# Kernel optimization log

Hardware: AMD Instinct MI355X
Metric: run time of the kernel (lower is better)

The kernel has to match this reference:

```python
import jax, jax.numpy as jnp
import numpy as np

N_NODES = 50000
N_EDGES = 800000
IN_F, HID_F, OUT_F = 256, 128, 64
NEG_SLOPE = 0.2
EPS = 1e-16


def _aggregate_with_attention(x, src, tgt, a_w, a_b, num_nodes):
    # x: [N, d]; src/tgt: [E]; a_w: [2d]; a_b: [1]
    d = x.shape[-1]
    x_src = x[src]                                   # [E, d] gather
    # att(cat([x_src, x_tgt])) == x_src @ a_w[:d] + x_tgt @ a_w[d:] + b
    alpha = x_src @ a_w[:d] + x[tgt] @ a_w[d:] + a_b[0]   # [E]
    alpha = jnp.where(alpha >= 0, alpha, NEG_SLOPE * alpha)  # leaky_relu(0.2)
    # segment softmax over edges grouped by target node
    m = jax.ops.segment_max(alpha, tgt, num_segments=num_nodes)   # [N]
    e = jnp.exp(alpha - m[tgt])                                    # [E]
    s = jax.ops.segment_sum(e, tgt, num_segments=num_nodes)       # [N]
    alpha = e / (s[tgt] + EPS)                                     # [E]
    msgs = x_src * alpha[:, None]                                  # [E, d]
    return jax.ops.segment_sum(msgs, tgt, num_segments=num_nodes)  # [N, d]


def setup_inputs() -> dict:
    key = jax.random.key(0)
    ks = jax.random.split(key, 10)
    x = jax.random.normal(ks[0], (N_NODES, IN_F), dtype=jnp.float32)
    edge_index = jax.random.randint(ks[1], (2, N_EDGES), 0, N_NODES, dtype=jnp.int32)
    sc1 = 1.0 / np.sqrt(IN_F)
    sc2 = 1.0 / np.sqrt(HID_F)
    return {
        "x": x,
        "edge_index": edge_index,
        "W1": jax.random.normal(ks[2], (IN_F, HID_F), dtype=jnp.float32) * sc1,
        "b1": jax.random.normal(ks[3], (HID_F,), dtype=jnp.float32) * sc1,
        "a1_w": jax.random.normal(ks[4], (2 * HID_F,), dtype=jnp.float32) * sc2,
        "a1_b": jax.random.normal(ks[5], (1,), dtype=jnp.float32) * sc2,
        "W2": jax.random.normal(ks[6], (HID_F, OUT_F), dtype=jnp.float32) * sc2,
        "b2": jax.random.normal(ks[7], (OUT_F,), dtype=jnp.float32) * sc2,
        "a2_w": jax.random.normal(ks[8], (2 * OUT_F,), dtype=jnp.float32) * (1.0 / np.sqrt(OUT_F)),
        "a2_b": jax.random.normal(ks[9], (1,), dtype=jnp.float32) * (1.0 / np.sqrt(OUT_F)),
    }


def reference(x, edge_index, W1, b1, a1_w, a1_b, W2, b2, a2_w, a2_b):
    src, tgt = edge_index[0], edge_index[1]
    n = x.shape[0]
    # eval mode: dropout is identity
    h = jax.nn.elu(x @ W1 + b1)                           # [N, HID]
    h = _aggregate_with_attention(h, src, tgt, a1_w, a1_b, n)
    o = h @ W2 + b2                                        # [N, OUT]
    o = _aggregate_with_attention(o, src, tgt, a2_w, a2_b, n)
    return jax.nn.log_softmax(o, axis=-1)
```

## Files before the change

kernel.cpp:

```cpp
#include <hip/hip_runtime.h>

#define NN    50000
#define NE    800000
#define INF_  256
#define HIDF  128
#define OUTF  64
#define NBUCK 196
#define CAP   5120
#define CHUNK 2048
#define NPART1 ((NE + CHUNK - 1) / CHUNK)
#define NLIN1B ((NN + 127) / 128)
#define NLIN2B ((NN + 127) / 128)
#define NPREP  160

typedef unsigned int uint;
typedef unsigned short ushort;
typedef __attribute__((ext_vector_type(8))) short short8;
typedef __attribute__((ext_vector_type(4))) float float4v;

__device__ __forceinline__ short f2bf(float f) {
    union { float f; unsigned u; } v; v.f = f;
    unsigned r = v.u + 0x7fffu + ((v.u >> 16) & 1u);
    return (short)(r >> 16);
}
__device__ __forceinline__ float bflo(uint u) {
    union { uint u; float f; } v; v.u = u << 16; return v.f;
}
__device__ __forceinline__ float bfhi(uint u) {
    union { uint u; float f; } v; v.u = u & 0xffff0000u; return v.f;
}

__device__ __forceinline__ int excl_scan256(int v, int* ws) {
    int lane = threadIdx.x & 63, wv = threadIdx.x >> 6;
    int x = v;
    #pragma unroll
    for (int o = 1; o < 64; o <<= 1) {
        int y = __shfl_up(x, o);
        if (lane >= o) x += y;
    }
    if (lane == 63) ws[wv] = x;
    __syncthreads();
    int add = 0;
    #pragma unroll
    for (int w = 0; w < 4; w++) add += (w < wv) ? ws[w] : 0;
    return x + add - v;
}

__device__ __forceinline__ int excl_scan512(int v, int* ws) {
    int lane = threadIdx.x & 63, wv = threadIdx.x >> 6;
    int x = v;
    #pragma unroll
    for (int o = 1; o < 64; o <<= 1) {
        int y = __shfl_up(x, o);
        if (lane >= o) x += y;
    }
    if (lane == 63) ws[wv] = x;
    __syncthreads();
    int add = 0;
    #pragma unroll
    for (int w = 0; w < 8; w++) add += (w < wv) ? ws[w] : 0;
    return x + add - v;
}

__global__ __launch_bounds__(256) void k_prep(const float* __restrict__ W1, const float* __restrict__ W2,
                                              short* __restrict__ W1f, short* __restrict__ W2f,
                                              int* __restrict__ bcur) {
    if (blockIdx.x == NPREP) {
        if (threadIdx.x < NBUCK) bcur[threadIdx.x] = 0;
        return;
    }
    int i = blockIdx.x * 256 + threadIdx.x;
    if (i < INF_ * HIDF) {
        int kk = i & 7, t = i >> 3;
        int m_l = t & 15, q = (t >> 4) & 3, s = t >> 6;
        int nb = s & 7, kc = s >> 3;
        int k = kc * 32 + q * 8 + kk, n = nb * 16 + m_l;
        W1f[i] = f2bf(W1[k * HIDF + n]);
    } else if (i < INF_ * HIDF + HIDF * OUTF) {
        int i2 = i - INF_ * HIDF;
        int kk = i2 & 7, t = i2 >> 3;
        int m_l = t & 15, q = (t >> 4) & 3, s = t >> 6;
        int nb = s & 3, kc = s >> 2;
        int k = kc * 32 + q * 8 + kk, n = nb * 16 + m_l;
        W2f[i2] = f2bf(W2[k * OUTF + n]);
    }
}


__global__ __launch_bounds__(256, 3) void k_f1(const int* __restrict__ src, const int* __restrict__ tgt,
                                               int* __restrict__ bcur, uint2* __restrict__ pairs,
                                               const float* __restrict__ X, const short* __restrict__ W1f,
                                               const float* __restrict__ b1, ushort* __restrict__ Hb,
                                               const float* __restrict__ a1w, float* __restrict__ s1s,
                                               float* __restrict__ s1t) {
    if (blockIdx.x < NPART1) {
        __shared__ int hist[NBUCK], lofs[NBUCK], cur[NBUCK], gstart[NBUCK];
        __shared__ int ws[4];
        __shared__ int ltgt[CHUNK], lsrc[CHUNK];
        int tid = threadIdx.x;
        for (int i = tid; i < NBUCK; i += 256) hist[i] = 0;
        __syncthreads();

        int base = blockIdx.x * CHUNK;
        int cnt = NE - base; if (cnt > CHUNK) cnt = CHUNK;

        int t_[8], s_[8];
        #pragma unroll
        for (int k = 0; k < 8; k++) {
            int idx = k * 256 + tid;
            if (idx < cnt) {
                int j = base + idx;
                t_[k] = tgt[j]; s_[k] = src[j];
                atomicAdd(&hist[t_[k] >> 8], 1);
            } else t_[k] = -1;
        }
        __syncthreads();

        int v = (tid < NBUCK) ? hist[tid] : 0;
        int excl = excl_scan256(v, ws);
        if (tid < NBUCK) {
            lofs[tid] = excl;
            cur[tid] = excl;
            gstart[tid] = atomicAdd(&bcur[tid], v);
        }
        __syncthreads();

        #pragma unroll
        for (int k = 0; k < 8; k++) {
            if (t_[k] >= 0) {
                int b = t_[k] >> 8;
                int pos = atomicAdd(&cur[b], 1);
                ltgt[pos] = t_[k]; lsrc[pos] = s_[k];
            }
        }
        __syncthreads();

        for (int j = tid; j < cnt; j += 256) {
            int tv = ltgt[j];
            int b = tv >> 8;
            int dst = gstart[b] + (j - lofs[b]);
            pairs[(size_t)b * CAP + dst] = make_uint2((uint)tv, (uint)lsrc[j]);
        }
        return;
    }
    int bid = blockIdx.x - NPART1;
    int w = threadIdx.x >> 6;
    int l = threadIdx.x & 63;
    int m_l = l & 15, q = l >> 4;
    int row0 = bid * 128 + w * 32;
    int rA0 = row0 + m_l;
    int rA1 = row0 + 16 + m_l;
    int rc0 = rA0 < NN ? rA0 : NN - 1;
    int rc1 = rA1 < NN ? rA1 : NN - 1;
    const float* pa0 = X + (size_t)rc0 * INF_ + q * 8;
    const float* pa1 = X + (size_t)rc1 * INF_ + q * 8;
    const short8* Bp = (const short8*)W1f;

    short8 af0[8], af1[8];
    #pragma unroll
    for (int kc = 0; kc < 8; kc++) {
        float4 u0 = *(const float4*)(pa0 + kc * 32);
        float4 u1 = *(const float4*)(pa0 + kc * 32 + 4);
        float4 v0 = *(const float4*)(pa1 + kc * 32);
        float4 v1 = *(const float4*)(pa1 + kc * 32 + 4);
        af0[kc][0] = f2bf(u0.x); af0[kc][1] = f2bf(u0.y); af0[kc][2] = f2bf(u0.z); af0[kc][3] = f2bf(u0.w);
        af0[kc][4] = f2bf(u1.x); af0[kc][5] = f2bf(u1.y); af0[kc][6] = f2bf(u1.z); af0[kc][7] = f2bf(u1.w);
        af1[kc][0] = f2bf(v0.x); af1[kc][1] = f2bf(v0.y); af1[kc][2] = f2bf(v0.z); af1[kc][3] = f2bf(v0.w);
        af1[kc][4] = f2bf(v1.x); af1[kc][5] = f2bf(v1.y); af1[kc][6] = f2bf(v1.z); af1[kc][7] = f2bf(v1.w);
    }

    float4v acc0[8] = {}, acc1[8] = {};
    #pragma unroll
    for (int kc = 0; kc < 8; kc++) {
        #pragma unroll
        for (int n = 0; n < 8; n++) {
            short8 b = Bp[(kc * 8 + n) * 64 + l];
            acc0[n] = __builtin_amdgcn_mfma_f32_16x16x32_bf16(af0[kc], b, acc0[n], 0, 0, 0);
            acc1[n] = __builtin_amdgcn_mfma_f32_16x16x32_bf16(af1[kc], b, acc1[n], 0, 0, 0);
        }
    }

    float vs_r[8], vt_r[8];
    #pragma unroll
    for (int r = 0; r < 8; r++) { vs_r[r] = 0.f; vt_r[r] = 0.f; }
    #pragma unroll
    for (int n = 0; n < 8; n++) {
        int col = n * 16 + m_l;
        float bias = b1[col];
        float aw0 = a1w[col], aw1 = a1w[HIDF + col];
        #pragma unroll
        for (int r = 0; r < 4; r++) {
            int row = row0 + q * 4 + r;
            float v = acc0[n][r] + bias;
            v = v > 0.f ? v : expm1f(v);
            vs_r[r] += v * aw0; vt_r[r] += v * aw1;
            if (row < NN) Hb[(size_t)row * HIDF + col] = (ushort)f2bf(v);

            int row1 = row0 + 16 + q * 4 + r;
            float v1 = acc1[n][r] + bias;
            v1 = v1 > 0.f ? v1 : expm1f(v1);
            vs_r[4 + r] += v1 * aw0; vt_r[4 + r] += v1 * aw1;
            if (row1 < NN) Hb[(size_t)row1 * HIDF + col] = (ushort)f2bf(v1);
        }
    }
    #pragma unroll
    for (int r = 0; r < 8; r++) {
        #pragma unroll
        for (int o = 1; o < 16; o <<= 1) {
            vs_r[r] += __shfl_xor(vs_r[r], o);
            vt_r[r] += __shfl_xor(vt_r[r], o);
        }
    }
    if (m_l == 0) {
        #pragma unroll
        for (int r = 0; r < 4; r++) {
            int row = row0 + q * 4 + r;
            if (row < NN) { s1s[row] = vs_r[r]; s1t[row] = vt_r[r]; }
            int row1 = row0 + 16 + q * 4 + r;
            if (row1 < NN) { s1s[row1] = vs_r[4 + r]; s1t[row1] = vt_r[4 + r]; }
        }
    }
}

__global__ __launch_bounds__(512) void k_part2(const int* __restrict__ bcur, const uint2* __restrict__ pairs,
                                               int* __restrict__ fsrc, int* __restrict__ nbeg,
                                               int* __restrict__ ncnt) {
    __shared__ int hist[256], cur[256];
    __shared__ int ws[8];
    int tid = threadIdx.x;
    int b = blockIdx.x;
    int cnt = __builtin_amdgcn_readfirstlane(bcur[b]);
    if (tid < 256) hist[tid] = 0;
    __syncthreads();

    const uint2* pb = pairs + (size_t)b * CAP;
    for (int j = tid; j < cnt; j += 512) {
        uint2 e = pb[j];
        atomicAdd(&hist[e.x & 255], 1);
    }
    __syncthreads();

    int v = (tid < 256) ? hist[tid] : 0;
    int excl = excl_scan512(v, ws);
    if (tid < 256) {
        int node = (b << 8) + tid;
        if (node < NN) { nbeg[node] = b * CAP + excl; ncnt[node] = v; }
        cur[tid] = excl;
    }
    __syncthreads();

    for (int j = tid; j < cnt; j += 512) {
        uint2 e = pb[j];
        int pos = atomicAdd(&cur[e.x & 255], 1);
        fsrc[(size_t)b * CAP + pos] = (int)e.y;
    }
}

__global__ __launch_bounds__(256, 3) void k_linear2(const short* __restrict__ Hin, const short* __restrict__ W2f,
                                                    const float* __restrict__ b2, ushort* __restrict__ Ob,
                                                    const float* __restrict__ a2w, float* __restrict__ s2s,
                                                    float* __restrict__ s2t) {
    int w = threadIdx.x >> 6;
    int l = threadIdx.x & 63;
    int m_l = l & 15, q = l >> 4;
    int row0 = blockIdx.x * 128 + w * 32;
    int rA0 = row0 + m_l;
    int rA1 = row0 + 16 + m_l;
    int rc0 = rA0 < NN ? rA0 : NN - 1;
    int rc1 = rA1 < NN ? rA1 : NN - 1;
    const short* pa0 = Hin + (size_t)rc0 * HIDF + q * 8;
    const short* pa1 = Hin + (size_t)rc1 * HIDF + q * 8;
    const short8* Bp = (const short8*)W2f;

    short8 af0[4], af1[4];
    #pragma unroll
    for (int kc = 0; kc < 4; kc++) {
        af0[kc] = *(const short8*)(pa0 + kc * 32);
        af1[kc] = *(const short8*)(pa1 + kc * 32);
    }

    float4v acc0[4] = {}, acc1[4] = {};
    #pragma unroll
    for (int kc = 0; kc < 4; kc++) {
        #pragma unroll
        for (int n = 0; n < 4; n++) {
            short8 b = Bp[(kc * 4 + n) * 64 + l];
            acc0[n] = __builtin_amdgcn_mfma_f32_16x16x32_bf16(af0[kc], b, acc0[n], 0, 0, 0);
            acc1[n] = __builtin_amdgcn_mfma_f32_16x16x32_bf16(af1[kc], b, acc1[n], 0, 0, 0);
        }
    }

    float vs_r[8], vt_r[8];
    #pragma unroll
    for (int r = 0; r < 8; r++) { vs_r[r] = 0.f; vt_r[r] = 0.f; }
    #pragma unroll
    for (int n = 0; n < 4; n++) {
        int col = n * 16 + m_l;
        float bias = b2[col];
        float aw0 = a2w[col], aw1 = a2w[OUTF + col];
        #pragma unroll
        for (int r = 0; r < 4; r++) {
            int row = row0 + q * 4 + r;
            float v = acc0[n][r] + bias;
            vs_r[r] += v * aw0; vt_r[r] += v * aw1;
            if (row < NN) Ob[(size_t)row * OUTF + col] = (ushort)f2bf(v);

            int row1 = row0 + 16 + q * 4 + r;
            float v1 = acc1[n][r] + bias;
            vs_r[4 + r] += v1 * aw0; vt_r[4 + r] += v1 * aw1;
            if (row1 < NN) Ob[(size_t)row1 * OUTF + col] = (ushort)f2bf(v1);
        }
    }
    #pragma unroll
    for (int r = 0; r < 8; r++) {
        #pragma unroll
        for (int o = 1; o < 16; o <<= 1) {
            vs_r[r] += __shfl_xor(vs_r[r], o);
            vt_r[r] += __shfl_xor(vt_r[r], o);
        }
    }
    if (m_l == 0) {
        #pragma unroll
        for (int r = 0; r < 4; r++) {
            int row = row0 + q * 4 + r;
            if (row < NN) { s2s[row] = vs_r[r]; s2t[row] = vt_r[r]; }
            int row1 = row0 + 16 + q * 4 + r;
            if (row1 < NN) { s2s[row1] = vs_r[4 + r]; s2t[row1] = vt_r[4 + r]; }
        }
    }
}


__global__ __launch_bounds__(256) void k_agg1f(const uint* __restrict__ Hb4, const int* __restrict__ nbeg,
                                               const int* __restrict__ ncnt, const int* __restrict__ fsrc,
                                               const float* __restrict__ ss, const float* __restrict__ st_,
                                               const float* __restrict__ ab, uint* __restrict__ Hagg4) {
    int wid  = (blockIdx.x * 256 + threadIdx.x) >> 6;
    int lane = threadIdx.x & 63;
    if (wid >= NN) return;
    int beg = __builtin_amdgcn_readfirstlane(nbeg[wid]);
    int deg = __builtin_amdgcn_readfirstlane(ncnt[wid]);
    int end = beg + deg;
    float bias = ab[0] + st_[wid];
    float ax = 0.f, ay = 0.f, bx = 0.f, by = 0.f;

    if (deg > 0 && deg <= 64) {
        int my_s = 0; float a = -INFINITY;
        if (lane < deg) {
            my_s = fsrc[beg + lane];
            float t = ss[my_s] + bias;
            a = t >= 0.f ? t : 0.2f * t;
        }
        float m = a;
        #pragma unroll
        for (int o = 32; o > 0; o >>= 1) m = fmaxf(m, __shfl_xor(m, o));
        float e = (lane < deg) ? __expf(a - m) : 0.f;
        float sum = e;
        #pragma unroll
        for (int o = 32; o > 0; o >>= 1) sum += __shfl_xor(sum, o);
        float p = e * (1.f / (sum + 1e-16f));
        int nfull8 = deg & ~7;
        int j = 0;
        if (nfull8 > 0) {
            float wA[8]; uint xA[8];
            #pragma unroll
            for (int u = 0; u < 8; u++) {
                int s = __shfl(my_s, u); wA[u] = __shfl(p, u);
                xA[u] = Hb4[(size_t)s * 64 + lane];
            }
            for (j = 8; j < nfull8; j += 8) {
                float wB[8]; uint xB[8];
                #pragma unroll
                for (int u = 0; u < 8; u++) {
                    int s = __shfl(my_s, j + u); wB[u] = __shfl(p, j + u);
                    xB[u] = Hb4[(size_t)s * 64 + lane];
                }
                #pragma unroll
                for (int u = 0; u < 8; u += 2) {
                    ax += wA[u] * bflo(xA[u]);         ay += wA[u] * bfhi(xA[u]);
                    bx += wA[u + 1] * bflo(xA[u + 1]); by += wA[u + 1] * bfhi(xA[u + 1]);
                }
                #pragma unroll
                for (int u = 0; u < 8; u++) { xA[u] = xB[u]; wA[u] = wB[u]; }
            }
            #pragma unroll
            for (int u = 0; u < 8; u += 2) {
                ax += wA[u] * bflo(xA[u]);         ay += wA[u] * bfhi(xA[u]);
                bx += wA[u + 1] * bflo(xA[u + 1]); by += wA[u + 1] * bfhi(xA[u + 1]);
            }
        }
        if (j < deg) {
            int rem = deg - j;
            int sA[8]; float wA[8]; uint xA[8];
            #pragma unroll
            for (int u = 0; u < 8; u++) { sA[u] = __shfl(my_s, j + u); wA[u] = __shfl(p, j + u); }
            #pragma unroll
            for (int u = 0; u < 8; u++) xA[u] = (u < rem) ? Hb4[(size_t)sA[u] * 64 + lane] : 0u;
            #pragma unroll
            for (int u = 0; u < 8; u += 2) {
                ax += wA[u] * bflo(xA[u]);         ay += wA[u] * bfhi(xA[u]);
                bx += wA[u + 1] * bflo(xA[u + 1]); by += wA[u + 1] * bfhi(xA[u + 1]);
            }
        }
    } else if (deg > 64) {
        float m = -INFINITY;
        for (int i = beg + lane; i < end; i += 64) {
            float t = ss[fsrc[i]] + bias;
            t = t >= 0.f ? t : 0.2f * t;
            m = fmaxf(m, t);
        }
        #pragma unroll
        for (int o = 32; o > 0; o >>= 1) m = fmaxf(m, __shfl_xor(m, o));
        float sum = 0.f;
        for (int i = beg + lane; i < end; i += 64) {
            float t = ss[fsrc[i]] + bias;
            t = t >= 0.f ? t : 0.2f * t;
            sum += __expf(t - m);
        }
        #pragma unroll
        for (int o = 32; o > 0; o >>= 1) sum += __shfl_xor(sum, o);
        float inv = 1.f / (sum + 1e-16f);
        for (int c = beg; c < end; c += 64) {
            int cnt = min(64, end - c);
            int my_s = 0; float p = 0.f;
            if (lane < cnt) {
                my_s = fsrc[c + lane];
                float t = ss[my_s] + bias;
                t = t >= 0.f ? t : 0.2f * t;
                p = __expf(t - m) * inv;
            }
            for (int j = 0; j < cnt; j += 4) {
                int s0 = __shfl(my_s, j),     s1 = __shfl(my_s, j + 1);
                int s2 = __shfl(my_s, j + 2), s3 = __shfl(my_s, j + 3);
                float w0 = __shfl(p, j),     w1 = __shfl(p, j + 1);
                float w2 = __shfl(p, j + 2), w3 = __shfl(p, j + 3);
                uint x0 = Hb4[(size_t)s0 * 64 + lane];
                uint x1 = Hb4[(size_t)s1 * 64 + lane];
                uint x2 = Hb4[(size_t)s2 * 64 + lane];
                uint x3 = Hb4[(size_t)s3 * 64 + lane];
                ax += w0 * bflo(x0); ay += w0 * bfhi(x0);
                bx += w1 * bflo(x1); by += w1 * bfhi(x1);
                ax += w2 * bflo(x2); ay += w2 * bfhi(x2);
                bx += w3 * bflo(x3); by += w3 * bfhi(x3);
            }
        }
    }
    float fx = ax + bx, fy = ay + by;
    uint outv = (uint)(ushort)f2bf(fx) | ((uint)(ushort)f2bf(fy) << 16);
    Hagg4[(size_t)wid * 64 + lane] = outv;
}

__global__ __launch_bounds__(256) void k_agg2f(const uint* __restrict__ Ob4, const int* __restrict__ nbeg,
                                               const int* __restrict__ ncnt, const int* __restrict__ fsrc,
                                               const float* __restrict__ ss, const float* __restrict__ st_,
                                               const float* __restrict__ ab, float* __restrict__ out) {
    int wid  = (blockIdx.x * 256 + threadIdx.x) >> 6;
    int lane = threadIdx.x & 63;
    if (wid >= NN) return;
    int half = lane >> 5, li = lane & 31;
    int beg = __builtin_amdgcn_readfirstlane(nbeg[wid]);
    int deg = __builtin_amdgcn_readfirstlane(ncnt[wid]);
    int end = beg + deg;
    float bias = ab[0] + st_[wid];
    float a0 = 0.f, a1 = 0.f;

    if (deg > 0 && deg <= 64) {
        int my_s = 0; float a = -INFINITY;
        if (lane < deg) {
            my_s = fsrc[beg + lane];
            float t = ss[my_s] + bias;
            a = t >= 0.f ? t : 0.2f * t;
        }
        float m = a;
        #pragma unroll
        for (int o = 32; o > 0; o >>= 1) m = fmaxf(m, __shfl_xor(m, o));
        float e = (lane < deg) ? __expf(a - m) : 0.f;
        float sum = e;
        #pragma unroll
        for (int o = 32; o > 0; o >>= 1) sum += __shfl_xor(sum, o);
        float p = e * (1.f / (sum + 1e-16f));
        int nfull8 = deg & ~7;
        int j = 0;
        if (nfull8 > 0) {
            float wA_[4]; uint xA_[4];
            #pragma unroll
            for (int u = 0; u < 4; u++) {
                int ei_ = 2 * u + half;
                int s = __shfl(my_s, ei_); wA_[u] = __shfl(p, ei_);
                xA_[u] = Ob4[(size_t)s * 32 + li];
            }
            for (j = 8; j < nfull8; j += 8) {
                float wB_[4]; uint xB_[4];
                #pragma unroll
                for (int u = 0; u < 4; u++) {
                    int ei_ = j + 2 * u + half;
                    int s = __shfl(my_s, ei_); wB_[u] = __shfl(p, ei_);
                    xB_[u] = Ob4[(size_t)s * 32 + li];
                }
                #pragma unroll
                for (int u = 0; u < 4; u++) { a0 += wA_[u] * bflo(xA_[u]); a1 += wA_[u] * bfhi(xA_[u]); }
                #pragma unroll
                for (int u = 0; u < 4; u++) { xA_[u] = xB_[u]; wA_[u] = wB_[u]; }
            }
            #pragma unroll
            for (int u = 0; u < 4; u++) { a0 += wA_[u] * bflo(xA_[u]); a1 += wA_[u] * bfhi(xA_[u]); }
        }
        if (j < deg) {
            int rem = deg - j;
            #pragma unroll
            for (int k = 0; k < 4; k++) {
                int eo = 2 * k + half;
                int ei_ = j + eo;
                int sx = __shfl(my_s, ei_);
                float wx = __shfl(p, ei_);
                uint xx = (eo < rem) ? Ob4[(size_t)sx * 32 + li] : 0u;
                a0 += wx * bflo(xx); a1 += wx * bfhi(xx);
            }
        }
    } else if (deg > 64) {
        float m = -INFINITY;
        for (int i = beg + lane; i < end; i += 64) {
            float t = ss[fsrc[i]] + bias;
            t = t >= 0.f ? t : 0.2f * t;
            m = fmaxf(m, t);
        }
        #pragma unroll
        for (int o = 32; o > 0; o >>= 1) m = fmaxf(m, __shfl_xor(m, o));
        float sum = 0.f;
        for (int i = beg + lane; i < end; i += 64) {
            float t = ss[fsrc[i]] + bias;
            t = t >= 0.f ? t : 0.2f * t;
            sum += __expf(t - m);
        }
        #pragma unroll
        for (int o = 32; o > 0; o >>= 1) sum += __shfl_xor(sum, o);
        float inv = 1.f / (sum + 1e-16f);
        for (int c = beg; c < end; c += 64) {
            int cnt = min(64, end - c);
            int my_s = 0; float p = 0.f;
            if (lane < cnt) {
                my_s = fsrc[c + lane];
                float t = ss[my_s] + bias;
                t = t >= 0.f ? t : 0.2f * t;
                p = __expf(t - m) * inv;
            }
            for (int j = 0; j < cnt; j += 4) {
                int e0 = j + half, e1 = j + 2 + half;
                int s0 = __shfl(my_s, e0), s1 = __shfl(my_s, e1);
                float w0 = __shfl(p, e0), w1 = __shfl(p, e1);
                uint x0 = Ob4[(size_t)s0 * 32 + li];
                uint x1 = Ob4[(size_t)s1 * 32 + li];
                a0 += w0 * bflo(x0); a1 += w0 * bfhi(x0);
                a0 += w1 * bflo(x1); a1 += w1 * bfhi(x1);
            }
        }
    }
    a0 += __shfl_xor(a0, 32);
    a1 += __shfl_xor(a1, 32);
    float mx = fmaxf(a0, a1);
    #pragma unroll
    for (int o = 16; o > 0; o >>= 1) mx = fmaxf(mx, __shfl_xor(mx, o));
    float es = __expf(a0 - mx) + __expf(a1 - mx);
    #pragma unroll
    for (int o = 16; o > 0; o >>= 1) es += __shfl_xor(es, o);
    float lg = __logf(es);
    if (half == 0) {
        float2 r; r.x = a0 - mx - lg; r.y = a1 - mx - lg;
        ((float2*)out)[(size_t)wid * 32 + li] = r;
    }
}


extern "C" void kernel_launch(void* const* d_in, const int* in_sizes, int n_in,
                              void* d_out, int out_size, void* d_ws, size_t ws_size,
                              hipStream_t stream) {
    const float* X   = (const float*)d_in[0];
    const int*   ei  = (const int*)d_in[1];
    const float* W1  = (const float*)d_in[2];
    const float* b1  = (const float*)d_in[3];
    const float* a1w = (const float*)d_in[4];
    const float* a1b = (const float*)d_in[5];
    const float* W2  = (const float*)d_in[6];
    const float* b2  = (const float*)d_in[7];
    const float* a2w = (const float*)d_in[8];
    const float* a2b = (const float*)d_in[9];
    const int* src = ei;
    const int* tgt = ei + NE;

    char* p = (char*)d_ws;
    size_t off = 0;
    auto alloc = [&](size_t bytes) -> char* {
        char* r = p + off;
        off = (off + bytes + 255) & ~(size_t)255;
        return r;
    };
    ushort* Hb    = (ushort*)alloc((size_t)NN * HIDF * 2);
    ushort* Hagg  = (ushort*)alloc((size_t)NN * HIDF * 2);
    ushort* Ob    = (ushort*)alloc((size_t)NN * OUTF * 2);
    short* W1f    = (short*)alloc((size_t)INF_ * HIDF * 2);
    short* W2f    = (short*)alloc((size_t)HIDF * OUTF * 2);
    float* s1s    = (float*)alloc((size_t)NN * 4);
    float* s1t    = (float*)alloc((size_t)NN * 4);
    float* s2s    = (float*)alloc((size_t)NN * 4);
    float* s2t    = (float*)alloc((size_t)NN * 4);
    int*   bcur   = (int*)alloc((size_t)NBUCK * 4);
    uint2* pairs  = (uint2*)alloc((size_t)NBUCK * CAP * 8);
    int*   fsrc   = (int*)alloc((size_t)NBUCK * CAP * 4);
    int*   nbeg   = (int*)alloc((size_t)NN * 4);
    int*   ncnt   = (int*)alloc((size_t)NN * 4);

    k_prep   <<<NPREP + 1, 256, 0, stream>>>(W1, W2, W1f, W2f, bcur);
    k_f1     <<<NPART1 + NLIN1B, 256, 0, stream>>>(src, tgt, bcur, pairs,
                                                   X, W1f, b1, Hb, a1w, s1s, s1t);
    k_part2  <<<NBUCK, 512, 0, stream>>>(bcur, pairs, fsrc, nbeg, ncnt);
    k_agg1f  <<<NN / 4, 256, 0, stream>>>((const uint*)Hb, nbeg, ncnt, fsrc, s1s, s1t, a1b, (uint*)Hagg);
    k_linear2<<<NLIN2B, 256, 0, stream>>>((const short*)Hagg, W2f, b2, Ob, a2w, s2s, s2t);
    k_agg2f  <<<NN / 4, 256, 0, stream>>>((const uint*)Ob, nbeg, ncnt, fsrc, s2s, s2t, a2b, (float*)d_out);
}
```

Before: 209.2 us.

## Fuse layer-1 attention aggregation with second linear layer via LDS tile

Merges the layer-1 aggregation kernel and the second linear kernel into one kernel. Each block aggregates 16 nodes (4 per wave) into a bf16 tile in shared memory, then runs a 16x64 MFMA against W2 and writes Ob and the layer-2 attention scores. This drops the Hagg round trip through global memory and one kernel launch. In exchange each wave handles four nodes one after another, and the block barrier makes waves wait for the slowest node, which may lower latency hiding during the gather.

```diff
diff --git a/kernel.cpp b/kernel.cpp
--- a/kernel.cpp
+++ b/kernel.cpp
@@ -10,7 +10,7 @@
 #define CHUNK 2048
 #define NPART1 ((NE + CHUNK - 1) / CHUNK)
 #define NLIN1B ((NN + 127) / 128)
-#define NLIN2B ((NN + 127) / 128)
+#define NAGG1  (NN / 16)
 #define NPREP  160
 
 typedef unsigned int uint;
@@ -256,63 +256,158 @@
     }
 }
 
-__global__ __launch_bounds__(256, 3) void k_linear2(const short* __restrict__ Hin, const short* __restrict__ W2f,
-                                                    const float* __restrict__ b2, ushort* __restrict__ Ob,
-                                                    const float* __restrict__ a2w, float* __restrict__ s2s,
-                                                    float* __restrict__ s2t) {
-    int w = threadIdx.x >> 6;
-    int l = threadIdx.x & 63;
-    int m_l = l & 15, q = l >> 4;
-    int row0 = blockIdx.x * 128 + w * 32;
-    int rA0 = row0 + m_l;
-    int rA1 = row0 + 16 + m_l;
-    int rc0 = rA0 < NN ? rA0 : NN - 1;
-    int rc1 = rA1 < NN ? rA1 : NN - 1;
-    const short* pa0 = Hin + (size_t)rc0 * HIDF + q * 8;
-    const short* pa1 = Hin + (size_t)rc1 * HIDF + q * 8;
+
+__global__ __launch_bounds__(256) void k_agg1l2(const uint* __restrict__ Hb4, const int* __restrict__ nbeg,
+                                                const int* __restrict__ ncnt, const int* __restrict__ fsrc,
+                                                const float* __restrict__ ss, const float* __restrict__ st_,
+                                                const float* __restrict__ ab,
+                                                const short* __restrict__ W2f, const float* __restrict__ b2,
+                                                const float* __restrict__ a2w,
+                                                ushort* __restrict__ Ob, float* __restrict__ s2s,
+                                                float* __restrict__ s2t) {
+    __shared__ uint tile[16 * 68];
+    __shared__ float sAcc[4][16], sTcc[4][16];
+    int wv   = threadIdx.x >> 6;
+    int lane = threadIdx.x & 63;
+
+    #pragma unroll 1
+    for (int it = 0; it < 4; ++it) {
+        int wid = blockIdx.x * 16 + wv * 4 + it;
+        int beg = __builtin_amdgcn_readfirstlane(nbeg[wid]);
+        int deg = __builtin_amdgcn_readfirstlane(ncnt[wid]);
+        int end = beg + deg;
+        float bias = ab[0] + st_[wid];
+        float ax = 0.f, ay = 0.f, bx = 0.f, by = 0.f;
+
+        if (deg > 0 && deg <= 64) {
+            int my_s = 0; float a = -INFINITY;
+            if (lane < deg) {
+                my_s = fsrc[beg + lane];
+                float t = ss[my_s] + bias;
+                a = t >= 0.f ? t : 0.2f * t;
+            }
+            float m = a;
+            #pragma unroll
+            for (int o = 32; o > 0; o >>= 1) m = fmaxf(m, __shfl_xor(m, o));
+            float e = (lane < deg) ? __expf(a - m) : 0.f;
+            float sum = e;
+            #pragma unroll
+            for (int o = 32; o > 0; o >>= 1) sum += __shfl_xor(sum, o);
+            float p = e * (1.f / (sum + 1e-16f));
+            int nfull8 = deg & ~7;
+            int j = 0;
+            if (nfull8 > 0) {
+                float wA[8]; uint xA[8];
+                #pragma unroll
+                for (int u = 0; u < 8; u++) {
+                    int s = __shfl(my_s, u); wA[u] = __shfl(p, u);
+                    xA[u] = Hb4[(size_t)s * 64 + lane];
+                }
+                for (j = 8; j < nfull8; j += 8) {
+                    float wB[8]; uint xB[8];
+                    #pragma unroll
+                    for (int u = 0; u < 8; u++) {
+                        int s = __shfl(my_s, j + u); wB[u] = __shfl(p, j + u);
+                        xB[u] = Hb4[(size_t)s * 64 + lane];
+                    }
+                    #pragma unroll
+                    for (int u = 0; u < 8; u += 2) {
+                        ax += wA[u] * bflo(xA[u]);         ay += wA[u] * bfhi(xA[u]);
+                        bx += wA[u + 1] * bflo(xA[u + 1]); by += wA[u + 1] * bfhi(xA[u + 1]);
+                    }
+                    #pragma unroll
+                    for (int u = 0; u < 8; u++) { xA[u] = xB[u]; wA[u] = wB[u]; }
+                }
+                #pragma unroll
+                for (int u = 0; u < 8; u += 2) {
+                    ax += wA[u] * bflo(xA[u]);         ay += wA[u] * bfhi(xA[u]);
+                    bx += wA[u + 1] * bflo(xA[u + 1]); by += wA[u + 1] * bfhi(xA[u + 1]);
+                }
+            }
+            if (j < deg) {
+                int rem = deg - j;
+                int sA[8]; float wA[8]; uint xA[8];
+                #pragma unroll
+                for (int u = 0; u < 8; u++) { sA[u] = __shfl(my_s, j + u); wA[u] = __shfl(p, j + u); }
+                #pragma unroll
+                for (int u = 0; u < 8; u++) xA[u] = (u < rem) ? Hb4[(size_t)sA[u] * 64 + lane] : 0u;
+                #pragma unroll
+                for (int u = 0; u < 8; u += 2) {
+                    ax += wA[u] * bflo(xA[u]);         ay += wA[u] * bfhi(xA[u]);
+                    bx += wA[u + 1] * bflo(xA[u + 1]); by += wA[u + 1] * bfhi(xA[u + 1]);
+                }
+            }
+        } else if (deg > 64) {
+            float m = -INFINITY;
+            for (int i = beg + lane; i < end; i += 64) {
+                float t = ss[fsrc[i]] + bias;
+                t = t >= 0.f ? t : 0.2f * t;
+                m = fmaxf(m, t);
+            }
+            #pragma unroll
+            for (int o = 32; o > 0; o >>= 1) m = fmaxf(m, __shfl_xor(m, o));
+            float sum = 0.f;
+            for (int i = beg + lane; i < end; i += 64) {
+                float t = ss[fsrc[i]] + bias;
+                t = t >= 0.f ? t : 0.2f * t;
+                sum += __expf(t - m);
+            }
+            #pragma unroll
+            for (int o = 32; o > 0; o >>= 1) sum += __shfl_xor(sum, o);
+            float inv = 1.f / (sum + 1e-16f);
+            for (int c = beg; c < end; c += 64) {
+                int cnt = min(64, end - c);
+                int my_s = 0; float p = 0.f;
+                if (lane < cnt) {
+                    my_s = fsrc[c + lane];
+                    float t = ss[my_s] + bias;
+                    t = t >= 0.f ? t : 0.2f * t;
+                    p = __expf(t - m) * inv;
+                }
+                for (int j = 0; j < cnt; j += 4) {
+                    int s0 = __shfl(my_s, j),     s1 = __shfl(my_s, j + 1);
+                    int s2 = __shfl(my_s, j + 2), s3 = __shfl(my_s, j + 3);
+                    float w0 = __shfl(p, j),     w1 = __shfl(p, j + 1);
+                    float w2 = __shfl(p, j + 2), w3 = __shfl(p, j + 3);
+                    uint x0 = Hb4[(size_t)s0 * 64 + lane];
+                    uint x1 = Hb4[(size_t)s1 * 64 + lane];
+                    uint x2 = Hb4[(size_t)s2 * 64 + lane];
+                    uint x3 = Hb4[(size_t)s3 * 64 + lane];
+                    ax += w0 * bflo(x0); ay += w0 * bfhi(x0);
+                    bx += w1 * bflo(x1); by += w1 * bfhi(x1);
+                    ax += w2 * bflo(x2); ay += w2 * bfhi(x2);
+                    bx += w3 * bflo(x3); by += w3 * bfhi(x3);
+                }
+            }
+        }
+        float fx = ax + bx, fy = ay + by;
+        uint outv = (uint)(ushort)f2bf(fx) | ((uint)(ushort)f2bf(fy) << 16);
+        tile[(wv * 4 + it) * 68 + lane] = outv;
+    }
+    __syncthreads();
+
+    int m_l = lane & 15, q = lane >> 4;
     const short8* Bp = (const short8*)W2f;
-
-    short8 af0[4], af1[4];
+    float4v acc = {};
     #pragma unroll
     for (int kc = 0; kc < 4; kc++) {
-        af0[kc] = *(const short8*)(pa0 + kc * 32);
-        af1[kc] = *(const short8*)(pa1 + kc * 32);
-    }
-
-    float4v acc0[4] = {}, acc1[4] = {};
-    #pragma unroll
-    for (int kc = 0; kc < 4; kc++) {
-        #pragma unroll
-        for (int n = 0; n < 4; n++) {
-            short8 b = Bp[(kc * 4 + n) * 64 + l];
-            acc0[n] = __builtin_amdgcn_mfma_f32_16x16x32_bf16(af0[kc], b, acc0[n], 0, 0, 0);
-            acc1[n] = __builtin_amdgcn_mfma_f32_16x16x32_bf16(af1[kc], b, acc1[n], 0, 0, 0);
-        }
-    }
-
-    float vs_r[8], vt_r[8];
-    #pragma unroll
-    for (int r = 0; r < 8; r++) { vs_r[r] = 0.f; vt_r[r] = 0.f; }
-    #pragma unroll
-    for (int n = 0; n < 4; n++) {
-        int col = n * 16 + m_l;
-        float bias = b2[col];
-        float aw0 = a2w[col], aw1 = a2w[OUTF + col];
-        #pragma unroll
-        for (int r = 0; r < 4; r++) {
-            int row = row0 + q * 4 + r;
-            float v = acc0[n][r] + bias;
-            vs_r[r] += v * aw0; vt_r[r] += v * aw1;
-            if (row < NN) Ob[(size_t)row * OUTF + col] = (ushort)f2bf(v);
-
-            int row1 = row0 + 16 + q * 4 + r;
-            float v1 = acc1[n][r] + bias;
-            vs_r[4 + r] += v1 * aw0; vt_r[4 + r] += v1 * aw1;
-            if (row1 < NN) Ob[(size_t)row1 * OUTF + col] = (ushort)f2bf(v1);
-        }
-    }
-    #pragma unroll
-    for (int r = 0; r < 8; r++) {
+        short8 afr = *(const short8*)&tile[m_l * 68 + kc * 16 + q * 4];
+        short8 b = Bp[(kc * 4 + wv) * 64 + lane];
+        acc = __builtin_amdgcn_mfma_f32_16x16x32_bf16(afr, b, acc, 0, 0, 0);
+    }
+    int col = wv * 16 + m_l;
+    float bias2 = b2[col];
+    float aw0 = a2w[col], aw1 = a2w[OUTF + col];
+    float vs_r[4], vt_r[4];
+    #pragma unroll
+    for (int r = 0; r < 4; r++) {
+        int row = q * 4 + r;
+        float v = acc[r] + bias2;
+        vs_r[r] = v * aw0; vt_r[r] = v * aw1;
+        Ob[(size_t)(blockIdx.x * 16 + row) * OUTF + col] = (ushort)f2bf(v);
+    }
+    #pragma unroll
+    for (int r = 0; r < 4; r++) {
         #pragma unroll
         for (int o = 1; o < 16; o <<= 1) {
             vs_r[r] += __shfl_xor(vs_r[r], o);
@@ -321,134 +416,16 @@
     }
     if (m_l == 0) {
         #pragma unroll
-        for (int r = 0; r < 4; r++) {
-            int row = row0 + q * 4 + r;
-            if (row < NN) { s2s[row] = vs_r[r]; s2t[row] = vt_r[r]; }
-            int row1 = row0 + 16 + q * 4 + r;
-            if (row1 < NN) { s2s[row1] = vs_r[4 + r]; s2t[row1] = vt_r[4 + r]; }
-        }
-    }
-}
-
-
-__global__ __launch_bounds__(256) void k_agg1f(const uint* __restrict__ Hb4, const int* __restrict__ nbeg,
-                                               const int* __restrict__ ncnt, const int* __restrict__ fsrc,
-                                               const float* __restrict__ ss, const float* __restrict__ st_,
-                                               const float* __restrict__ ab, uint* __restrict__ Hagg4) {
-    int wid  = (blockIdx.x * 256 + threadIdx.x) >> 6;
-    int lane = threadIdx.x & 63;
-    if (wid >= NN) return;
-    int beg = __builtin_amdgcn_readfirstlane(nbeg[wid]);
-    int deg = __builtin_amdgcn_readfirstlane(ncnt[wid]);
-    int end = beg + deg;
-    float bias = ab[0] + st_[wid];
-    float ax = 0.f, ay = 0.f, bx = 0.f, by = 0.f;
-
-    if (deg > 0 && deg <= 64) {
-        int my_s = 0; float a = -INFINITY;
-        if (lane < deg) {
-            my_s = fsrc[beg + lane];
-            float t = ss[my_s] + bias;
-            a = t >= 0.f ? t : 0.2f * t;
-        }
-        float m = a;
-        #pragma unroll
-        for (int o = 32; o > 0; o >>= 1) m = fmaxf(m, __shfl_xor(m, o));
-        float e = (lane < deg) ? __expf(a - m) : 0.f;
-        float sum = e;
-        #pragma unroll
-        for (int o = 32; o > 0; o >>= 1) sum += __shfl_xor(sum, o);
-        float p = e * (1.f / (sum + 1e-16f));
-        int nfull8 = deg & ~7;
-        int j = 0;
-        if (nfull8 > 0) {
-            float wA[8]; uint xA[8];
-            #pragma unroll
-            for (int u = 0; u < 8; u++) {
-                int s = __shfl(my_s, u); wA[u] = __shfl(p, u);
-                xA[u] = Hb4[(size_t)s * 64 + lane];
-            }
-            for (j = 8; j < nfull8; j += 8) {
-                float wB[8]; uint xB[8];
-                #pragma unroll
-                for (int u = 0; u < 8; u++) {
-                    int s = __shfl(my_s, j + u); wB[u] = __shfl(p, j + u);
-                    xB[u] = Hb4[(size_t)s * 64 + lane];
-                }
-                #pragma unroll
-                for (int u = 0; u < 8; u += 2) {
-                    ax += wA[u] * bflo(xA[u]);         ay += wA[u] * bfhi(xA[u]);
-                    bx += wA[u + 1] * bflo(xA[u + 1]); by += wA[u + 1] * bfhi(xA[u + 1]);
-                }
-                #pragma unroll
-                for (int u = 0; u < 8; u++) { xA[u] = xB[u]; wA[u] = wB[u]; }
-            }
-            #pragma unroll
-            for (int u = 0; u < 8; u += 2) {
-                ax += wA[u] * bflo(xA[u]);         ay += wA[u] * bfhi(xA[u]);
-                bx += wA[u + 1] * bflo(xA[u + 1]); by += wA[u + 1] * bfhi(xA[u + 1]);
-            }
-        }
-        if (j < deg) {
-            int rem = deg - j;
-            int sA[8]; float wA[8]; uint xA[8];
-            #pragma unroll
-            for (int u = 0; u < 8; u++) { sA[u] = __shfl(my_s, j + u); wA[u] = __shfl(p, j + u); }
-            #pragma unroll
-            for (int u = 0; u < 8; u++) xA[u] = (u < rem) ? Hb4[(size_t)sA[u] * 64 + lane] : 0u;
-            #pragma unroll
-            for (int u = 0; u < 8; u += 2) {
-                ax += wA[u] * bflo(xA[u]);         ay += wA[u] * bfhi(xA[u]);
-                bx += wA[u + 1] * bflo(xA[u + 1]); by += wA[u + 1] * bfhi(xA[u + 1]);
-            }
-        }
-    } else if (deg > 64) {
-        float m = -INFINITY;
-        for (int i = beg + lane; i < end; i += 64) {
-            float t = ss[fsrc[i]] + bias;
-            t = t >= 0.f ? t : 0.2f * t;
-            m = fmaxf(m, t);
-        }
-        #pragma unroll
-        for (int o = 32; o > 0; o >>= 1) m = fmaxf(m, __shfl_xor(m, o));
-        float sum = 0.f;
-        for (int i = beg + lane; i < end; i += 64) {
-            float t = ss[fsrc[i]] + bias;
-            t = t >= 0.f ? t : 0.2f * t;
-            sum += __expf(t - m);
-        }
-        #pragma unroll
-        for (int o = 32; o > 0; o >>= 1) sum += __shfl_xor(sum, o);
-        float inv = 1.f / (sum + 1e-16f);
-        for (int c = beg; c < end; c += 64) {
-            int cnt = min(64, end - c);
-            int my_s = 0; float p = 0.f;
-            if (lane < cnt) {
-                my_s = fsrc[c + lane];
-                float t = ss[my_s] + bias;
-                t = t >= 0.f ? t : 0.2f * t;
-                p = __expf(t - m) * inv;
-            }
-            for (int j = 0; j < cnt; j += 4) {
-                int s0 = __shfl(my_s, j),     s1 = __shfl(my_s, j + 1);
-                int s2 = __shfl(my_s, j + 2), s3 = __shfl(my_s, j + 3);
-                float w0 = __shfl(p, j),     w1 = __shfl(p, j + 1);
-                float w2 = __shfl(p, j + 2), w3 = __shfl(p, j + 3);
-                uint x0 = Hb4[(size_t)s0 * 64 + lane];
-                uint x1 = Hb4[(size_t)s1 * 64 + lane];
-                uint x2 = Hb4[(size_t)s2 * 64 + lane];
-                uint x3 = Hb4[(size_t)s3 * 64 + lane];
-                ax += w0 * bflo(x0); ay += w0 * bfhi(x0);
-                bx += w1 * bflo(x1); by += w1 * bfhi(x1);
-                ax += w2 * bflo(x2); ay += w2 * bfhi(x2);
-                bx += w3 * bflo(x3); by += w3 * bfhi(x3);
-            }
-        }
-    }
-    float fx = ax + bx, fy = ay + by;
-    uint outv = (uint)(ushort)f2bf(fx) | ((uint)(ushort)f2bf(fy) << 16);
-    Hagg4[(size_t)wid * 64 + lane] = outv;
-}
+        for (int r = 0; r < 4; r++) { sAcc[wv][q * 4 + r] = vs_r[r]; sTcc[wv][q * 4 + r] = vt_r[r]; }
+    }
+    __syncthreads();
+    if (threadIdx.x < 16) {
+        int row = threadIdx.x;
+        s2s[blockIdx.x * 16 + row] = sAcc[0][row] + sAcc[1][row] + sAcc[2][row] + sAcc[3][row];
+        s2t[blockIdx.x * 16 + row] = sTcc[0][row] + sTcc[1][row] + sTcc[2][row] + sTcc[3][row];
+    }
+}
+
 
 __global__ __launch_bounds__(256) void k_agg2f(const uint* __restrict__ Ob4, const int* __restrict__ nbeg,
                                                const int* __restrict__ ncnt, const int* __restrict__ fsrc,
@@ -595,7 +572,6 @@
         return r;
     };
     ushort* Hb    = (ushort*)alloc((size_t)NN * HIDF * 2);
-    ushort* Hagg  = (ushort*)alloc((size_t)NN * HIDF * 2);
     ushort* Ob    = (ushort*)alloc((size_t)NN * OUTF * 2);
     short* W1f    = (short*)alloc((size_t)INF_ * HIDF * 2);
     short* W2f    = (short*)alloc((size_t)HIDF * OUTF * 2);
@@ -613,7 +589,7 @@
     k_f1     <<<NPART1 + NLIN1B, 256, 0, stream>>>(src, tgt, bcur, pairs,
                                                    X, W1f, b1, Hb, a1w, s1s, s1t);
     k_part2  <<<NBUCK, 512, 0, stream>>>(bcur, pairs, fsrc, nbeg, ncnt);
-    k_agg1f  <<<NN / 4, 256, 0, stream>>>((const uint*)Hb, nbeg, ncnt, fsrc, s1s, s1t, a1b, (uint*)Hagg);
-    k_linear2<<<NLIN2B, 256, 0, stream>>>((const short*)Hagg, W2f, b2, Ob, a2w, s2s, s2t);
+    k_agg1l2 <<<NAGG1, 256, 0, stream>>>((const uint*)Hb, nbeg, ncnt, fsrc, s1s, s1t, a1b,
+                                         W2f, b2, a2w, Ob, s2s, s2t);
     k_agg2f  <<<NN / 4, 256, 0, stream>>>((const uint*)Ob, nbeg, ncnt, fsrc, s2s, s2t, a2b, (float*)d_out);
 }
```

Measured after the change: 210.9 us. No clear change (+0.8%).
